# Kernel optimization log

Measured on AMD Instinct MI355X. Metric: run time of the kernel, lower is better.

## Reference

```python
import jax, jax.numpy as jnp
import numpy as np

NUM_FRAMES = 8
NUM_HEADS = 12
NEG = -1e9


def _masks(N):
    i = jnp.arange(N)[:, None]
    j = jnp.arange(N)[None, :]
    b = NUM_FRAMES + 1  # boundary = 9
    head = (i < b) & (j < b)
    body = ((i >= b) & (j >= b)) | ((i == 0) & (j >= b)) | ((i >= b) & (j == 0)) | ((i == 0) & (j == 0))
    interact = ((i >= b) & (j < b)) | ((i < b) & (j >= b)) | ((i == 0) & (j == 0))
    return head, body, interact


def setup_inputs() -> dict:
    key = jax.random.key(0)
    k1, k2, k3 = jax.random.split(key, 3)
    B, N, C = 8, 1024, 768
    x = jax.random.normal(k1, (B, N, C), dtype=jnp.float32)
    w_qkv = jax.random.normal(k2, (3 * C, C), dtype=jnp.float32) * 0.02
    w_proj = jax.random.normal(k3, (C, C), dtype=jnp.float32) * 0.02
    b_proj = jnp.zeros((C,), dtype=jnp.float32)
    return {"x": x, "w_qkv": w_qkv, "w_proj": w_proj, "b_proj": b_proj}


def reference(x, w_qkv, w_proj, b_proj):
    B, N, C = x.shape
    H = NUM_HEADS
    hd = C // H
    scale = hd ** (-0.5)

    qkv = (x @ w_qkv.T).reshape(B, N, 3, H, hd).transpose(2, 0, 3, 1, 4)  # [3,B,H,N,hd]
    q, k, v = qkv[0], qkv[1], qkv[2]

    attn = jnp.einsum("bhnd,bhmd->bhnm", q, k) * scale  # [B,H,N,N]

    head_m, body_m, inter_m = _masks(N)

    def branch(mask):
        scores = jnp.where(mask, attn, NEG)
        p = jax.nn.softmax(scores, axis=-1)
        o = jnp.einsum("bhnm,bhmd->bhnd", p, v)  # [B,H,N,hd]
        o = o.transpose(0, 2, 1, 3).reshape(B, N, C)
        return o @ w_proj.T + b_proj

    return branch(head_m), branch(body_m), branch(inter_m)
```

## Files before the change

### kernel.cpp

```cpp
#include <hip/hip_runtime.h>
#include <stdint.h>

typedef unsigned short u16;
typedef unsigned int u32;
using f32x4 = __attribute__((ext_vector_type(4))) float;
using bf16x8 = __attribute__((ext_vector_type(8))) short;
using u16x8 = __attribute__((ext_vector_type(8))) unsigned short;
using u16x4 = __attribute__((ext_vector_type(4))) unsigned short;
using u32x2 = __attribute__((ext_vector_type(2))) unsigned int;

#define QSCALE 0.18033688f

__device__ __forceinline__ u16 f2bf(float f) {
  u32 u = __float_as_uint(f);
  u32 r = (u + 0x7FFFu + ((u >> 16) & 1u)) >> 16;
  return (u16)r;
}
__device__ __forceinline__ float bf2f(u16 h) { return __uint_as_float(((u32)h) << 16); }

__device__ __forceinline__ u32 pack_trunc(float lo, float hi) {
  return (__float_as_uint(hi) & 0xFFFF0000u) | (__float_as_uint(lo) >> 16);
}

__device__ __forceinline__ void gload16(const void* g, void* l) {
  __builtin_amdgcn_global_load_lds((const __attribute__((address_space(1))) void*)g,
                                   (__attribute__((address_space(3))) void*)l, 16, 0, 0);
}

__global__ __launch_bounds__(256) void cvt3_kernel(const float* __restrict__ a, u16* __restrict__ da, int n4a,
                                                   const float* __restrict__ b, u16* __restrict__ db, int n4b,
                                                   const float* __restrict__ c, u16* __restrict__ dc, int n4c) {
  int i = blockIdx.x * 256 + threadIdx.x;
  const float* src;
  u16* dst;
  int n;
  if (i < n4a) {
    src = a; dst = da; n = i;
  } else if (i < n4a + n4b) {
    src = b; dst = db; n = i - n4a;
  } else if (i < n4a + n4b + n4c) {
    src = c; dst = dc; n = i - n4a - n4b;
  } else {
    return;
  }
  const float4 f = ((const float4*)src)[n];
  u16x4 o;
  o[0] = f2bf(f.x); o[1] = f2bf(f.y); o[2] = f2bf(f.z); o[3] = f2bf(f.w);
  ((u16x4*)dst)[n] = o;
}

template <int MODE, int Mdim, int Ndim, int Kdim>
__global__ __launch_bounds__(256) void gemm_bt(const u16* __restrict__ A, const u16* __restrict__ Bw,
                                               u16* __restrict__ qb, u16* __restrict__ kb,
                                               u16* __restrict__ vTb,
                                               float* __restrict__ out, const float* __restrict__ bias) {
  __shared__ __align__(16) u16 lA[2][128 * 32];
  __shared__ __align__(16) u16 lB[2][128 * 32];
  const int tid = threadIdx.x;
  const int wid = tid >> 6, lane = tid & 63;
  const int m0 = blockIdx.x * 128, n0 = blockIdx.y * 128;
  const int wm = (wid >> 1) * 64, wn = (wid & 1) * 64;
  const int g = lane >> 4, r16 = lane & 15;

  f32x4 acc[4][4] = {};

  const int srow = wid * 16 + (lane >> 2);
  const int scol = (lane & 3) * 8;
  const u16* gA = A + (size_t)(m0 + srow) * Kdim + scol;
  const u16* gB = Bw + (size_t)(n0 + srow) * Kdim + scol;

  gload16(gA, lA[0] + wid * 512);
  gload16(gA + (size_t)64 * Kdim, lA[0] + wid * 512 + 2048);
  gload16(gB, lB[0] + wid * 512);
  gload16(gB + (size_t)64 * Kdim, lB[0] + wid * 512 + 2048);
  __syncthreads();

  int cur = 0;
  for (int k0 = 0; k0 < Kdim; k0 += 32) {
    if (k0 + 32 < Kdim) {
      const int nk = k0 + 32;
      u16* lAn = lA[cur ^ 1] + wid * 512;
      u16* lBn = lB[cur ^ 1] + wid * 512;
      gload16(gA + nk, lAn);
      gload16(gA + (size_t)64 * Kdim + nk, lAn + 2048);
      gload16(gB + nk, lBn);
      gload16(gB + (size_t)64 * Kdim + nk, lBn + 2048);
    }
    const u16* lAc = lA[cur];
    const u16* lBc = lB[cur];
    bf16x8 af[4], bfr[4];
#pragma unroll
    for (int i = 0; i < 4; ++i) af[i] = *(const bf16x8*)(lAc + (wm + i * 16 + r16) * 32 + g * 8);
#pragma unroll
    for (int j = 0; j < 4; ++j) bfr[j] = *(const bf16x8*)(lBc + (wn + j * 16 + r16) * 32 + g * 8);
#pragma unroll
    for (int i = 0; i < 4; ++i)
#pragma unroll
      for (int j = 0; j < 4; ++j)
        acc[i][j] = __builtin_amdgcn_mfma_f32_16x16x32_bf16(af[i], bfr[j], acc[i][j], 0, 0, 0);
    __syncthreads();
    cur ^= 1;
  }

#pragma unroll
  for (int i = 0; i < 4; ++i) {
    const int gm = m0 + wm + i * 16 + g * 4;
#pragma unroll
    for (int j = 0; j < 4; ++j) {
      const int gn = n0 + wn + j * 16 + r16;
      if constexpr (MODE == 1) {
        const float bv = bias[gn];
#pragma unroll
        for (int r = 0; r < 4; ++r) out[(size_t)(gm + r) * Ndim + gn] = acc[i][j][r] + bv;
      } else {
        const int t = gn / 768;
        const int rem = gn - t * 768;
        const int h = rem >> 6, d = rem & 63;
        if (t == 2) {
          u16x4 pk;
#pragma unroll
          for (int r = 0; r < 4; ++r) pk[r] = f2bf(acc[i][j][r]);
          const int b = gm >> 10, n = gm & 1023;
          *(u16x4*)(vTb + ((size_t)((b * 12 + h) * 64 + d)) * 1024 + n) = pk;
        } else {
          u16* dst = (t == 0) ? qb : kb;
          const float sc = (t == 0) ? QSCALE : 1.0f;
#pragma unroll
          for (int r = 0; r < 4; ++r) {
            const int b = (gm + r) >> 10, n = (gm + r) & 1023;
            dst[((size_t)((b * 12 + h) * 1024 + n)) * 64 + d] = f2bf(acc[i][j][r] * sc);
          }
        }
      }
    }
  }
}

__global__ __launch_bounds__(256) void vmean_kernel(const u16* __restrict__ vTb,
                                                    float* __restrict__ vmean) {
  const int bh = blockIdx.x, t = threadIdx.x;
  const int d = t >> 2, part = t & 3;
  const u16* src = vTb + ((size_t)bh * 64 + d) * 1024 + part * 256;
  float s = 0.f;
  for (int j = 0; j < 256; j += 8) {
    u16x8 u = *(const u16x8*)(src + j);
#pragma unroll
    for (int e = 0; e < 8; ++e) s += bf2f(u[e]);
  }
  s += __shfl_xor(s, 1);
  s += __shfl_xor(s, 2);
  if (part == 0) vmean[bh * 64 + d] = s * (1.0f / 1024.0f);
}

__global__ __launch_bounds__(256) void body_attn(const u16* __restrict__ qg, const u16* __restrict__ kg,
                                                 const u16* __restrict__ vg, const float* __restrict__ vmean,
                                                 u16* __restrict__ og) {
  __shared__ __align__(16) u16 lK[2][64 * 64];
  __shared__ __align__(16) u16 lV[2][64 * 64];
  __shared__ __align__(16) u16 lP[4][16 * 72];

  const int blk = blockIdx.x;
  const int gid = (blk & 7) * 192 + (blk >> 3);
  const int rt = gid & 15, bh = gid >> 4;
  const int tid = threadIdx.x, wid = tid >> 6, lane = tid & 63;
  const int g = lane >> 4, r16 = lane & 15;
  const int row0 = rt * 64 + wid * 16;

  const u16* qrow = qg + ((size_t)bh * 1024 + row0 + r16) * 64;
  const bf16x8 aq0 = *(const bf16x8*)(qrow + g * 8);
  const bf16x8 aq1 = *(const bf16x8*)(qrow + 32 + g * 8);

  const int lrow = lane >> 3, lch = lane & 7;
  const int swz = (lch ^ lrow) * 8;
  const int j0 = wid * 2;
  const u16* gK = kg + (size_t)bh * 65536 + (size_t)(j0 * 8 + lrow) * 64 + swz;
  const u16* gV = vg + (size_t)bh * 65536 + (size_t)(j0 * 8 + lrow) * 1024 + swz;

  f32x4 oa[4] = {};
  f32x4 osum = {};
  u16* lPw = lP[wid];

  bf16x8 vones;
#pragma unroll
  for (int i = 0; i < 8; ++i) vones[i] = (short)0x3F80;

  auto stage = [&](int c0, int buf) {
    gload16(gK + (size_t)c0 * 64, lK[buf] + j0 * 512);
    gload16(gK + (size_t)c0 * 64 + 512, lK[buf] + (j0 + 1) * 512);
    gload16(gV + c0, lV[buf] + j0 * 512);
    gload16(gV + c0 + 8192, lV[buf] + (j0 + 1) * 512);
  };

  auto compute = [&](const u16* lKc, const u16* lVc, int c0) {
#pragma unroll
    for (int kt = 0; kt < 4; ++kt) {
      const int key = kt * 16 + r16;
      const bf16x8 bk0 = *(const bf16x8*)(lKc + key * 64 + ((g ^ (key & 7)) * 8));
      const bf16x8 bk1 = *(const bf16x8*)(lKc + key * 64 + (((4 + g) ^ (key & 7)) * 8));
      f32x4 S = {};
      S = __builtin_amdgcn_mfma_f32_16x16x32_bf16(bk0, aq0, S, 0, 0, 0);
      S = __builtin_amdgcn_mfma_f32_16x16x32_bf16(bk1, aq1, S, 0, 0, 0);
      float p[4];
#pragma unroll
      for (int r = 0; r < 4; ++r) p[r] = exp2f(S[r]);
      if (c0 == 0 && kt == 0) {
        const int q = row0 + r16;
        const bool dropk0 = (q >= 1 && q <= 8);
#pragma unroll
        for (int r = 0; r < 4; ++r) {
          const int k = 4 * g + r;
          const bool keep = (k >= 9) || (k == 0 && !dropk0);
          p[r] = keep ? p[r] : 0.f;
        }
      }
      u32x2 w;
      w[0] = pack_trunc(p[0], p[1]);
      w[1] = pack_trunc(p[2], p[3]);
      *(u32x2*)((char*)lPw + r16 * 144 + kt * 32 + g * 8) = w;
    }
#pragma unroll
    for (int m = 0; m < 2; ++m) {
      const bf16x8 ap = *(const bf16x8*)((char*)lPw + r16 * 144 + m * 64 + g * 16);
#pragma unroll
      for (int jt = 0; jt < 4; ++jt) {
        const int d = jt * 16 + r16;
        const bf16x8 bv = *(const bf16x8*)(lVc + d * 64 + (((m * 4 + g) ^ (d & 7)) * 8));
        oa[jt] = __builtin_amdgcn_mfma_f32_16x16x32_bf16(ap, bv, oa[jt], 0, 0, 0);
      }
      osum = __builtin_amdgcn_mfma_f32_16x16x32_bf16(ap, vones, osum, 0, 0, 0);
    }
  };

  stage(0, 0);
  __syncthreads();

  for (int it = 0; it < 8; ++it) {
    const int c0 = it * 128;
    stage(c0 + 64, 1);
    compute(lK[0], lV[0], c0);
    __syncthreads();
    if (it < 7) stage(c0 + 128, 0);
    compute(lK[1], lV[1], c0 + 64);
    __syncthreads();
  }

  const int b = bh / 12, h = bh - b * 12;
#pragma unroll
  for (int r = 0; r < 4; ++r) {
    const int grow = row0 + 4 * g + r;
    const bool full = (grow >= 1 && grow <= 8);
    const float inv = 1.f / osum[r];
#pragma unroll
    for (int jt = 0; jt < 4; ++jt) {
      const int d = jt * 16 + r16;
      const float vi = oa[jt][r] * inv;
      const float vb = full ? vmean[bh * 64 + d] : vi;
      og[((size_t)(8192 + b * 1024 + grow)) * 768 + h * 64 + d] = f2bf(vb);
      if (grow <= 8)
        og[((size_t)(16384 + b * 1024 + grow)) * 768 + h * 64 + d] = f2bf(vi);
    }
  }
}

__global__ __launch_bounds__(256) void smalls_attn(const u16* __restrict__ qg, const u16* __restrict__ kg,
                                                   const u16* __restrict__ vg, const float* __restrict__ vmean,
                                                   u16* __restrict__ og) {
  __shared__ __align__(16) u16 lP2[4][16 * 40];
  __shared__ float lsRed[4][16];
  const int bh = blockIdx.y;
  const int b = bh / 12, h = bh - b * 12;
  const int tid = threadIdx.x, wid = tid >> 6, lane = tid & 63;
  const int g = lane >> 4, r16 = lane & 15;
  u16* lPw = lP2[wid];

  const int row0 = blockIdx.x * 64 + wid * 16;
  const u16* qrow = qg + ((size_t)bh * 1024 + row0 + r16) * 64;
  const bf16x8 aq0 = *(const bf16x8*)(qrow + g * 8);
  const bf16x8 aq1 = *(const bf16x8*)(qrow + 32 + g * 8);
  const u16* krow = kg + ((size_t)bh * 1024 + r16) * 64;
  const bf16x8 bk0 = *(const bf16x8*)(krow + g * 8);
  const bf16x8 bk1 = *(const bf16x8*)(krow + 32 + g * 8);
  f32x4 S = {};
  S = __builtin_amdgcn_mfma_f32_16x16x32_bf16(bk0, aq0, S, 0, 0, 0);
  S = __builtin_amdgcn_mfma_f32_16x16x32_bf16(bk1, aq1, S, 0, 0, 0);
  float p[4];
  float lsum = 0.f;
#pragma unroll
  for (int r = 0; r < 4; ++r) {
    const int k = 4 * g + r;
    p[r] = (k < 9) ? exp2f(S[r]) : 0.f;
    lsum += p[r];
  }
  {
    u16x4 pk;
#pragma unroll
    for (int r = 0; r < 4; ++r) pk[r] = f2bf(p[r]);
    *(u16x4*)((char*)lPw + r16 * 80 + g * 8) = pk;
    u16x4 z = {0, 0, 0, 0};
    *(u16x4*)((char*)lPw + r16 * 80 + 32 + g * 8) = z;
  }
  lsum += __shfl_xor(lsum, 16);
  lsum += __shfl_xor(lsum, 32);
  if (lane < 16) lsRed[wid][lane] = lsum;
  const bf16x8 ap = *(const bf16x8*)((char*)lPw + r16 * 80 + g * 16);
  f32x4 oa[4] = {};
#pragma unroll
  for (int jt = 0; jt < 4; ++jt) {
    const u16* vrow = vg + ((size_t)bh * 64 + jt * 16 + r16) * 1024;
    const bf16x8 bv = *(const bf16x8*)(vrow + g * 8);
    oa[jt] = __builtin_amdgcn_mfma_f32_16x16x32_bf16(ap, bv, oa[jt], 0, 0, 0);
  }
#pragma unroll
  for (int r = 0; r < 4; ++r) {
    const int grow = row0 + 4 * g + r;
    const float inv = 1.f / lsRed[wid][4 * g + r];
#pragma unroll
    for (int jt = 0; jt < 4; ++jt) {
      const int d = jt * 16 + r16;
      const float v = oa[jt][r] * inv;
      if (grow >= 9) {
        og[((size_t)(16384 + b * 1024 + grow)) * 768 + h * 64 + d] = f2bf(v);
        og[((size_t)(b * 1024 + grow)) * 768 + h * 64 + d] = f2bf(vmean[bh * 64 + d]);
      } else {
        og[((size_t)(b * 1024 + grow)) * 768 + h * 64 + d] = f2bf(v);
      }
    }
  }
}

extern "C" void kernel_launch(void* const* d_in, const int* in_sizes, int n_in,
                              void* d_out, int out_size, void* d_ws, size_t ws_size,
                              hipStream_t stream) {
  (void)in_sizes; (void)n_in; (void)out_size; (void)ws_size;
  const float* x      = (const float*)d_in[0];
  const float* w_qkv  = (const float*)d_in[1];
  const float* w_proj = (const float*)d_in[2];
  const float* b_proj = (const float*)d_in[3];

  char* ws = (char*)d_ws;
  u16* xb     = (u16*)(ws + 0);
  u16* wqkvb  = (u16*)(ws + 12582912);
  u16* wprojb = (u16*)(ws + 16121856);
  u16* qb     = (u16*)(ws + 17301504);
  u16* kb     = (u16*)(ws + 29884416);
  u16* vTb    = (u16*)(ws + 42467328);
  float* vmn  = (float*)(ws + 55050240);
  u16* ob     = (u16*)(ws + 55074816);

  cvt3_kernel<<<8449, 256, 0, stream>>>(x, xb, 1572864, w_qkv, wqkvb, 442368, w_proj, wprojb, 147456);

  gemm_bt<0, 8192, 2304, 768><<<dim3(64, 18), 256, 0, stream>>>(
      xb, wqkvb, qb, kb, vTb, nullptr, nullptr);

  vmean_kernel<<<96, 256, 0, stream>>>(vTb, vmn);

  body_attn<<<1536, 256, 0, stream>>>(qb, kb, vTb, vmn, ob);
  smalls_attn<<<dim3(16, 96), 256, 0, stream>>>(qb, kb, vTb, vmn, ob);

  gemm_bt<1, 24576, 768, 768><<<dim3(192, 6), 256, 0, stream>>>(
      ob, wprojb, nullptr, nullptr, nullptr, (float*)d_out, b_proj);
}
```

Measured before the change: 181.6 us.

## Triple-buffer GEMM LDS tiles with partial vmcnt waits

Replaces the double-buffered LDS staging in the bf16 GEMM with a three-stage ring, issuing global-to-LDS loads two K-tiles ahead. Barriers now wait only for the oldest outstanding loads (vmcnt(4)) instead of draining all memory operations, so load latency can overlap more MFMA work. This raises LDS use per block from 32KB to 48KB, which may lower occupancy. Correctness depends on the counter-based waits matching the async LDS load ordering.

```diff
diff --git a/kernel.cpp b/kernel.cpp
--- a/kernel.cpp
+++ b/kernel.cpp
@@ -54,8 +54,8 @@
                                                u16* __restrict__ qb, u16* __restrict__ kb,
                                                u16* __restrict__ vTb,
                                                float* __restrict__ out, const float* __restrict__ bias) {
-  __shared__ __align__(16) u16 lA[2][128 * 32];
-  __shared__ __align__(16) u16 lB[2][128 * 32];
+  __shared__ __align__(16) u16 lA[3 * 128 * 32];
+  __shared__ __align__(16) u16 lB[3 * 128 * 32];
   const int tid = threadIdx.x;
   const int wid = tid >> 6, lane = tid & 63;
   const int m0 = blockIdx.x * 128, n0 = blockIdx.y * 128;
@@ -69,25 +69,31 @@
   const u16* gA = A + (size_t)(m0 + srow) * Kdim + scol;
   const u16* gB = Bw + (size_t)(n0 + srow) * Kdim + scol;
 
-  gload16(gA, lA[0] + wid * 512);
-  gload16(gA + (size_t)64 * Kdim, lA[0] + wid * 512 + 2048);
-  gload16(gB, lB[0] + wid * 512);
-  gload16(gB + (size_t)64 * Kdim, lB[0] + wid * 512 + 2048);
-  __syncthreads();
+  auto stage = [&](int t, int buf) {
+    const int k0 = t * 32;
+    u16* a = lA + buf * 4096 + wid * 512;
+    u16* b = lB + buf * 4096 + wid * 512;
+    gload16(gA + k0, a);
+    gload16(gA + (size_t)64 * Kdim + k0, a + 2048);
+    gload16(gB + k0, b);
+    gload16(gB + (size_t)64 * Kdim + k0, b + 2048);
+  };
+
+  constexpr int NT = Kdim / 32;
+  stage(0, 0);
+  stage(1, 1);
+  asm volatile("s_waitcnt vmcnt(4)" ::: "memory");
+  __builtin_amdgcn_s_barrier();
+  __builtin_amdgcn_sched_barrier(0);
 
   int cur = 0;
-  for (int k0 = 0; k0 < Kdim; k0 += 32) {
-    if (k0 + 32 < Kdim) {
-      const int nk = k0 + 32;
-      u16* lAn = lA[cur ^ 1] + wid * 512;
-      u16* lBn = lB[cur ^ 1] + wid * 512;
-      gload16(gA + nk, lAn);
-      gload16(gA + (size_t)64 * Kdim + nk, lAn + 2048);
-      gload16(gB + nk, lBn);
-      gload16(gB + (size_t)64 * Kdim + nk, lBn + 2048);
-    }
-    const u16* lAc = lA[cur];
-    const u16* lBc = lB[cur];
+  for (int t = 0; t < NT; ++t) {
+    int nx2 = cur + 2;
+    if (nx2 >= 3) nx2 -= 3;
+    if (t + 2 < NT) stage(t + 2, nx2);
+
+    const u16* lAc = lA + cur * 4096;
+    const u16* lBc = lB + cur * 4096;
     bf16x8 af[4], bfr[4];
 #pragma unroll
     for (int i = 0; i < 4; ++i) af[i] = *(const bf16x8*)(lAc + (wm + i * 16 + r16) * 32 + g * 8);
@@ -98,8 +104,17 @@
 #pragma unroll
       for (int j = 0; j < 4; ++j)
         acc[i][j] = __builtin_amdgcn_mfma_f32_16x16x32_bf16(af[i], bfr[j], acc[i][j], 0, 0, 0);
-    __syncthreads();
-    cur ^= 1;
+
+    if (t + 2 < NT) {
+      asm volatile("s_waitcnt vmcnt(4)" ::: "memory");
+      __builtin_amdgcn_s_barrier();
+      __builtin_amdgcn_sched_barrier(0);
+    } else if (t + 1 < NT) {
+      asm volatile("s_waitcnt vmcnt(0)" ::: "memory");
+      __builtin_amdgcn_s_barrier();
+      __builtin_amdgcn_sched_barrier(0);
+    }
+    cur = (cur + 1 == 3) ? 0 : cur + 1;
   }
 
 #pragma unroll
```

Result: no change. 184.9 us (+1.8%).

## Read K and V directly from global memory instead of LDS double-buffering

Applied to the files above, without the earlier changes.

Drops the shared-memory double-buffered staging of K and V tiles in the body attention kernel. Each wave now loads its MFMA operands straight from global memory and relies on L1/L2 caching. This removes the block-wide barriers and the LDS traffic, but every one of the four waves now fetches the same K/V data separately, and the loads are no longer prefetched ahead of compute.

```diff
diff --git a/kernel.cpp b/kernel.cpp
--- a/kernel.cpp
+++ b/kernel.cpp
@@ -155,8 +155,6 @@
 __global__ __launch_bounds__(256) void body_attn(const u16* __restrict__ qg, const u16* __restrict__ kg,
                                                  const u16* __restrict__ vg, const float* __restrict__ vmean,
                                                  u16* __restrict__ og) {
-  __shared__ __align__(16) u16 lK[2][64 * 64];
-  __shared__ __align__(16) u16 lV[2][64 * 64];
   __shared__ __align__(16) u16 lP[4][16 * 72];
 
   const int blk = blockIdx.x;
@@ -170,11 +168,8 @@
   const bf16x8 aq0 = *(const bf16x8*)(qrow + g * 8);
   const bf16x8 aq1 = *(const bf16x8*)(qrow + 32 + g * 8);
 
-  const int lrow = lane >> 3, lch = lane & 7;
-  const int swz = (lch ^ lrow) * 8;
-  const int j0 = wid * 2;
-  const u16* gK = kg + (size_t)bh * 65536 + (size_t)(j0 * 8 + lrow) * 64 + swz;
-  const u16* gV = vg + (size_t)bh * 65536 + (size_t)(j0 * 8 + lrow) * 1024 + swz;
+  const u16* kbh = kg + (size_t)bh * 65536;
+  const u16* vbh = vg + (size_t)bh * 65536;
 
   f32x4 oa[4] = {};
   f32x4 osum = {};
@@ -184,19 +179,12 @@
 #pragma unroll
   for (int i = 0; i < 8; ++i) vones[i] = (short)0x3F80;
 
-  auto stage = [&](int c0, int buf) {
-    gload16(gK + (size_t)c0 * 64, lK[buf] + j0 * 512);
-    gload16(gK + (size_t)c0 * 64 + 512, lK[buf] + (j0 + 1) * 512);
-    gload16(gV + c0, lV[buf] + j0 * 512);
-    gload16(gV + c0 + 8192, lV[buf] + (j0 + 1) * 512);
-  };
-
-  auto compute = [&](const u16* lKc, const u16* lVc, int c0) {
+  for (int c0 = 0; c0 < 1024; c0 += 64) {
 #pragma unroll
     for (int kt = 0; kt < 4; ++kt) {
-      const int key = kt * 16 + r16;
-      const bf16x8 bk0 = *(const bf16x8*)(lKc + key * 64 + ((g ^ (key & 7)) * 8));
-      const bf16x8 bk1 = *(const bf16x8*)(lKc + key * 64 + (((4 + g) ^ (key & 7)) * 8));
+      const u16* krow = kbh + (size_t)(c0 + kt * 16 + r16) * 64;
+      const bf16x8 bk0 = *(const bf16x8*)(krow + g * 8);
+      const bf16x8 bk1 = *(const bf16x8*)(krow + 32 + g * 8);
       f32x4 S = {};
       S = __builtin_amdgcn_mfma_f32_16x16x32_bf16(bk0, aq0, S, 0, 0, 0);
       S = __builtin_amdgcn_mfma_f32_16x16x32_bf16(bk1, aq1, S, 0, 0, 0);
@@ -223,25 +211,12 @@
       const bf16x8 ap = *(const bf16x8*)((char*)lPw + r16 * 144 + m * 64 + g * 16);
 #pragma unroll
       for (int jt = 0; jt < 4; ++jt) {
-        const int d = jt * 16 + r16;
-        const bf16x8 bv = *(const bf16x8*)(lVc + d * 64 + (((m * 4 + g) ^ (d & 7)) * 8));
+        const u16* vrow = vbh + (size_t)(jt * 16 + r16) * 1024 + c0 + m * 32 + g * 8;
+        const bf16x8 bv = *(const bf16x8*)vrow;
         oa[jt] = __builtin_amdgcn_mfma_f32_16x16x32_bf16(ap, bv, oa[jt], 0, 0, 0);
       }
       osum = __builtin_amdgcn_mfma_f32_16x16x32_bf16(ap, vones, osum, 0, 0, 0);
     }
-  };
-
-  stage(0, 0);
-  __syncthreads();
-
-  for (int it = 0; it < 8; ++it) {
-    const int c0 = it * 128;
-    stage(c0 + 64, 1);
-    compute(lK[0], lV[0], c0);
-    __syncthreads();
-    if (it < 7) stage(c0 + 128, 0);
-    compute(lK[1], lV[1], c0 + 64);
-    __syncthreads();
   }
 
   const int b = bh / 12, h = bh - b * 12;
```

Measured after the change: 301.4 us. +66.0%, slower.
